# Kernel tuning notes

Hardware: AMD Instinct MI355X
Metric: run time of the kernel (lower is better)

Reference implementation:

```python
import jax, jax.numpy as jnp
import numpy as np

CONF_THRES = 0.25
IOU_THRES = 0.45
MAX_DET = 300
MAX_WH = 4096.0  # class offset for class-aware (non-agnostic) NMS
B, N, NC = 16, 25200, 80


def setup_inputs() -> dict:
    key = jax.random.key(0)
    k1, k2 = jax.random.split(key)
    p = jax.random.uniform(k1, (B, N, 5 + NC), dtype=jnp.float32)
    # scale to realistic YOLO pixel-space xywh for a 640x640 image
    cx = p[..., 0] * 640.0
    cy = p[..., 1] * 640.0
    w = p[..., 2] * 96.0 + 4.0
    h = p[..., 3] * 96.0 + 4.0
    obj = p[..., 4]
    cls = p[..., 5:] * 0.9
    prediction = jnp.concatenate([jnp.stack([cx, cy, w, h, obj], axis=-1), cls], axis=-1)
    logits = jax.random.normal(k2, (B, N, NC), dtype=jnp.float32)
    return {"prediction": prediction, "logits": logits}


def xywh2xyxy(b):
    cx, cy, w, h = b[..., 0], b[..., 1], b[..., 2], b[..., 3]
    return jnp.stack([cx - w * 0.5, cy - h * 0.5, cx + w * 0.5, cy + h * 0.5], axis=-1)


def _iou_one_vs_all(box, boxes):
    # box: [4], boxes: [N,4] in xyxy
    lt = jnp.maximum(box[:2], boxes[:, :2])
    rb = jnp.minimum(box[2:], boxes[:, 2:])
    wh = jnp.clip(rb - lt, 0.0)
    inter = wh[:, 0] * wh[:, 1]
    a1 = (box[2] - box[0]) * (box[3] - box[1])
    a2 = (boxes[:, 2] - boxes[:, 0]) * (boxes[:, 3] - boxes[:, 1])
    return inter / (a1 + a2 - inter + 1e-9)


def _nms_image(x6, boxes_off, scores, log_):
    # greedy NMS, fixed MAX_DET iterations; suppressed/invalid scores are -1
    def step(s, _):
        best = jnp.argmax(s)
        keep = s[best] > 0.0
        iou = _iou_one_vs_all(boxes_off[best], boxes_off)
        s = jnp.where(iou > IOU_THRES, -1.0, s)  # also suppresses 'best' (IoU=1)
        return s, (best, keep)
    _, (idx, keep) = jax.lax.scan(step, scores, None, length=MAX_DET)
    km = keep.astype(x6.dtype)[:, None]
    dets = x6[idx] * km          # [MAX_DET, 6] zero-padded
    lg = log_[idx] * km          # [MAX_DET, 80]
    return dets, lg, keep


def reference(prediction, logits):
    obj = prediction[..., 4]                          # [B,N]
    cls_conf = prediction[..., 5:] * obj[..., None]   # x[:,5:] *= x[:,4:5]
    conf = jnp.max(cls_conf, axis=-1)                 # best class conf
    j = jnp.argmax(cls_conf, axis=-1)                 # best class index
    box = xywh2xyxy(prediction[..., :4])              # [B,N,4]
    valid = (obj > CONF_THRES) & (conf > CONF_THRES)
    scores = jnp.where(valid, conf, -1.0)
    boxes_off = box + (j.astype(box.dtype) * MAX_WH)[..., None]  # class-aware offset
    x6 = jnp.concatenate([box, conf[..., None], j.astype(box.dtype)[..., None]], axis=-1)
    dets, lg, keep = jax.vmap(_nms_image)(x6, boxes_off, scores, logits)
    return dets, lg, keep
```

## Files before the change

kernel.cpp:

```cpp
#include <hip/hip_runtime.h>
#include <cstdint>

#define BB 16
#define NN 25200
#define NCLS 80
#define ROW 85
#define MAXDET 300
#define HBINS 2048
#define CAP2 512
#define TGT 448
#define CONF_T 0.25f
#define IOU_T 0.45f
#define NT 1024

typedef float f4u __attribute__((ext_vector_type(4), aligned(4)));

static const size_t OFF_REC = 1612800;

__global__ __launch_bounds__(256) void k_pre(const float* __restrict__ pred,
                                             float* __restrict__ scoreArr,
                                             float4* __restrict__ recG) {
    int tid = threadIdx.x;
    int t = tid & 3;
    int row = blockIdx.x * 64 + (tid >> 2);
    const float* rp = pred + (size_t)row * ROW;
    float obj = rp[4];
    float best = -1.0f; int bc = 1 << 20;
    f4u c0v;
#pragma unroll
    for (int i = 0; i < 6; ++i) {
        int jj = t + 4 * i;
        if (jj < 21) {
            f4u v4 = *reinterpret_cast<const f4u*>(rp + 4 * jj);
            if (jj == 0) c0v = v4;
            int c0 = 4 * jj;
#pragma unroll
            for (int e = 0; e < 4; ++e) {
                int col = c0 + e;
                if (col >= 5) {
                    float v = __fmul_rn(v4[e], obj);
                    if (v > best) { best = v; bc = col; }
                }
            }
        }
    }
    if (t == 1) {
        float v = __fmul_rn(rp[84], obj);
        if (v > best) { best = v; bc = 84; }
    }
#pragma unroll
    for (int d = 1; d <= 2; d <<= 1) {
        float ob = __shfl_xor(best, d);
        int   oc = __shfl_xor(bc, d);
        if (ob > best || (ob == best && oc < bc)) { best = ob; bc = oc; }
    }
    if (t == 0) {
        bool valid = (obj > CONF_T) && (best > CONF_T);
        scoreArr[row] = valid ? best : -1.0f;
        float cx = c0v[0], cy = c0v[1], w = c0v[2], h = c0v[3];
        float hw = __fmul_rn(w, 0.5f), hh = __fmul_rn(h, 0.5f);
        float4 bb = make_float4(__fsub_rn(cx, hw), __fsub_rn(cy, hh),
                                __fadd_rn(cx, hw), __fadd_rn(cy, hh));
        int bj = bc - 5;
        recG[(size_t)row * 2]     = bb;
        recG[(size_t)row * 2 + 1] = make_float4(__uint_as_float((unsigned)bj), 0.f, 0.f, 0.f);
    }
}

__global__ __launch_bounds__(NT) void k_fused(const float4* __restrict__ recG,
                                              const float* __restrict__ scoreArr,
                                              const float* __restrict__ logits,
                                              float* __restrict__ out) {
    __shared__ union {
        struct { unsigned hist[HBINS]; unsigned csum[257]; } h;
        unsigned long long maskS[CAP2][8];
    } u;
    __shared__ unsigned long long keys[CAP2];
    __shared__ float4 cbox_s[CAP2];
    __shared__ float4 raw_s[CAP2];
    __shared__ unsigned ccls_s[CAP2];
    __shared__ unsigned long long maskT_s[8][64];
    __shared__ unsigned long long keepm_s[8];
    __shared__ unsigned kidx[64];
    __shared__ unsigned rowsrc_s[MAXDET];
    __shared__ int flags[2];
    __shared__ int s_kept;

    int b = blockIdx.x, tid = threadIdx.x;
    int lane = tid & 63;

    for (int k = tid; k < HBINS; k += NT) u.h.hist[k] = 0u;
    if (tid == 0) { flags[0] = 0; flags[1] = 0; }
    __syncthreads();

    float sreg[25];
#pragma unroll
    for (int t = 0; t < 25; ++t) {
        int n = tid + t * NT;
        float s = (n < NN) ? scoreArr[(size_t)b * NN + n] : -1.0f;
        sreg[t] = s;
        if (s > 0.0f) {
            unsigned key = (__float_as_uint(s) - 0x3E800000u) >> 13;
            if (key > HBINS - 1) key = HBINS - 1;
            atomicAdd(&u.h.hist[key], 1u);
        }
    }
    __syncthreads();

    if (tid < 256) {
        unsigned cs = 0;
#pragma unroll
        for (int t = 0; t < 8; ++t) cs += u.h.hist[tid * 8 + t];
        u.h.csum[tid] = cs;
    }
    __syncthreads();
    for (int off = 1; off < 256; off <<= 1) {
        unsigned v = 0, add = 0;
        if (tid < 256) {
            v = u.h.csum[tid];
            add = (tid + off < 256) ? u.h.csum[tid + off] : 0u;
        }
        __syncthreads();
        if (tid < 256) u.h.csum[tid] = v + add;
        __syncthreads();
    }
    if (tid < 256) {
        unsigned Sc = u.h.csum[tid];
        unsigned Sn = (tid < 255) ? u.h.csum[tid + 1] : 0u;
        if (Sc >= TGT && (tid == 255 || Sn < TGT)) {
            unsigned cum = Sn;
            int t = tid * 8;
            for (int k = tid * 8 + 7; k >= tid * 8; --k) {
                cum += u.h.hist[k];
                if (cum >= TGT) { t = k; break; }
            }
            flags[1] = t;
        }
    }
    __syncthreads();
    unsigned thr = (unsigned)flags[1];

#pragma unroll
    for (int t = 0; t < 25; ++t) {
        int n = tid + t * NT;
        float s = sreg[t];
        bool win = false;
        if (s > 0.0f) {
            unsigned key = (__float_as_uint(s) - 0x3E800000u) >> 13;
            if (key > HBINS - 1) key = HBINS - 1;
            win = (key >= thr);
        }
        unsigned long long m = __ballot(win);
        if (m) {
            int lead = __ffsll((long long)m) - 1;
            int base = 0;
            if (lane == lead) base = atomicAdd(&flags[0], __popcll(m));
            base = __shfl(base, lead);
            if (win) {
                int pos = base + __popcll(m & ((1ULL << lane) - 1ULL));
                if (pos < CAP2)
                    keys[pos] = ((unsigned long long)__float_as_uint(s) << 32)
                              | (unsigned long long)(0xFFFFFFFFu - (unsigned)n);
            }
        }
    }
    __syncthreads();
    int c = min(flags[0], CAP2);
    for (int p = tid; p < CAP2; p += NT)
        if (p >= c) keys[p] = 0ULL;
    __syncthreads();

    for (int k = 2; k <= CAP2; k <<= 1) {
        for (int j = k >> 1; j > 0; j >>= 1) {
            for (int i = tid; i < CAP2; i += NT) {
                int ixj = i ^ j;
                if (ixj > i) {
                    unsigned long long k1 = keys[i], k2 = keys[ixj];
                    bool sw = ((i & k) == 0) ? (k1 < k2) : (k1 > k2);
                    if (sw) { keys[i] = k2; keys[ixj] = k1; }
                }
            }
            __syncthreads();
        }
    }

    if (tid < CAP2) {
        int p = tid;
        if (p < c) {
            int n = (int)(0xFFFFFFFFu - (unsigned)keys[p]);
            size_t rb = ((size_t)b * NN + n) * 2;
            float4 bb = recG[rb];
            unsigned bj = __float_as_uint(recG[rb + 1].x);
            raw_s[p] = bb;
            float off = __fmul_rn((float)bj, 4096.0f);
            cbox_s[p] = make_float4(__fadd_rn(bb.x, off), __fadd_rn(bb.y, off),
                                    __fadd_rn(bb.z, off), __fadd_rn(bb.w, off));
            ccls_s[p] = bj;
        } else {
            raw_s[p]  = make_float4(0.f, 0.f, 0.f, 0.f);
            cbox_s[p] = make_float4(0.f, 0.f, 0.f, 0.f);
            ccls_s[p] = 0u;
        }
    }
    __syncthreads();

    for (int k = tid; k < CAP2 * 8; k += NT) {
        int i = k & (CAP2 - 1);
        int w = k >> 9;
        int jbase = w << 6;
        unsigned long long m = 0ULL;
        if (i < c && i < jbase + 63) {
            float4 ci = cbox_s[i];
            float a1 = __fmul_rn(__fsub_rn(ci.z, ci.x), __fsub_rn(ci.w, ci.y));
#pragma unroll 4
            for (int jj = 0; jj < 64; ++jj) {
                int j = jbase + jj;
                float4 cj = cbox_s[j];
                float ltx = fmaxf(ci.x, cj.x), lty = fmaxf(ci.y, cj.y);
                float rbx = fminf(ci.z, cj.z), rby = fminf(ci.w, cj.w);
                float ww = fmaxf(__fsub_rn(rbx, ltx), 0.0f);
                float hh = fmaxf(__fsub_rn(rby, lty), 0.0f);
                float inter = __fmul_rn(ww, hh);
                if (j > i && inter > 0.0f) {
                    float a2 = __fmul_rn(__fsub_rn(cj.z, cj.x), __fsub_rn(cj.w, cj.y));
                    float denom = __fadd_rn(__fsub_rn(__fadd_rn(a1, a2), inter), 1e-9f);
                    if (inter / denom > IOU_T) m |= (1ULL << jj);
                }
            }
        }
        u.maskS[i][w] = m;
    }
    if (tid < 512) {
        int w = tid >> 6, l = tid & 63;
        int jbase = w << 6, p = jbase + l;
        unsigned long long m = 0ULL;
        if (p < c) {
            float4 cl = cbox_s[p];
            float a2 = __fmul_rn(__fsub_rn(cl.z, cl.x), __fsub_rn(cl.w, cl.y));
            for (int ii = 0; ii < 64; ++ii) {
                float4 ci = cbox_s[jbase + ii];
                float ltx = fmaxf(ci.x, cl.x), lty = fmaxf(ci.y, cl.y);
                float rbx = fminf(ci.z, cl.z), rby = fminf(ci.w, cl.w);
                float ww = fmaxf(__fsub_rn(rbx, ltx), 0.0f);
                float hh = fmaxf(__fsub_rn(rby, lty), 0.0f);
                float inter = __fmul_rn(ww, hh);
                if (ii < l && inter > 0.0f) {
                    float a1 = __fmul_rn(__fsub_rn(ci.z, ci.x), __fsub_rn(ci.w, ci.y));
                    float denom = __fadd_rn(__fsub_rn(__fadd_rn(a1, a2), inter), 1e-9f);
                    if (inter / denom > IOU_T) m |= (1ULL << ii);
                }
            }
        }
        maskT_s[w][l] = m;
    }
    __syncthreads();

    if (tid < 64) {
        unsigned long long remq = 0ULL;
        int kept = 0;
        for (int w = 0; w < 8; ++w) {
            int base = w << 6;
            unsigned long long tw = __shfl(remq, w);
            bool pre = ((tw >> lane) & 1ULL) != 0ULL;
            bool validl = (base + lane) < c;
            unsigned long long Cl = maskT_s[w][lane];
            unsigned long long initK = __ballot(validl && !pre);
            unsigned long long K = initK;
            for (int it = 0; it < 64; ++it) {
                bool sup = (Cl & K & ((1ULL << lane) - 1ULL)) != 0ULL;
                unsigned long long K2 = initK & __ballot(!sup);
                if (K2 == K) break;
                K = K2;
            }
            int limit = MAXDET - kept;
            int nk = __popcll(K);
            if (nk > limit) {
                if (limit <= 0) K = 0ULL;
                else {
                    int pref = __popcll(K & ((2ULL << lane) - 1ULL));
                    bool el = ((K >> lane) & 1ULL) && (pref <= limit);
                    K = __ballot(el);
                }
            }
            kept += __popcll(K);
            if (lane == 0) keepm_s[w] = K;
            if (K != 0ULL && w < 7) {
                if ((K >> lane) & 1ULL) {
                    int r = __popcll(K & ((1ULL << lane) - 1ULL));
                    kidx[r] = (unsigned)lane;
                }
                __builtin_amdgcn_s_waitcnt(0);
                int nkk = __popcll(K);
                int q = lane & 7, slot = lane >> 3;
                unsigned long long acc = 0ULL;
                for (int t = slot; t < nkk; t += 8)
                    acc |= u.maskS[base + (int)kidx[t]][q];
                acc |= __shfl_xor(acc, 8);
                acc |= __shfl_xor(acc, 16);
                acc |= __shfl_xor(acc, 32);
                if (slot == 0) remq |= acc;
            }
        }
        if (lane == 0) s_kept = kept;
    }
    __syncthreads();
    int kept = s_kept;

    float* dets = out;
    float* lg   = out + (size_t)BB * MAXDET * 6;
    float* kpo  = lg  + (size_t)BB * MAXDET * NCLS;

    for (int p = tid; p < CAP2; p += NT) {
        if (p < c) {
            int w = p >> 6, bitp = p & 63;
            unsigned long long kw = keepm_s[w];
            if ((kw >> bitp) & 1ULL) {
                int rank = __popcll(kw & ((1ULL << bitp) - 1ULL));
                for (int q = 0; q < w; ++q) rank += __popcll(keepm_s[q]);
                if (rank < MAXDET) {
                    float4 bb = raw_s[p];
                    unsigned long long key = keys[p];
                    float* dr = dets + ((size_t)b * MAXDET + rank) * 6;
                    dr[0] = bb.x; dr[1] = bb.y; dr[2] = bb.z; dr[3] = bb.w;
                    dr[4] = __uint_as_float((unsigned)(key >> 32));
                    dr[5] = (float)ccls_s[p];
                    rowsrc_s[rank] = 0xFFFFFFFFu - (unsigned)key;
                }
            }
        }
    }
    for (int i = tid; i < MAXDET; i += NT) {
        if (i >= kept) {
            float* dr = dets + ((size_t)b * MAXDET + i) * 6;
#pragma unroll
            for (int q = 0; q < 6; ++q) dr[q] = 0.0f;
        }
        kpo[b * MAXDET + i] = (i < kept) ? 1.0f : 0.0f;
    }
    __syncthreads();
    {
        const int HC = NCLS / 2;
        for (int i2 = tid; i2 < MAXDET * HC; i2 += NT) {
            int t = i2 / HC, col2 = i2 - t * HC;
            float2 v = make_float2(0.f, 0.f);
            if (t < kept)
                v = *reinterpret_cast<const float2*>(
                        logits + ((size_t)b * NN + rowsrc_s[t]) * NCLS + col2 * 2);
            *reinterpret_cast<float2*>(
                lg + (size_t)b * MAXDET * NCLS + (size_t)t * NCLS + col2 * 2) = v;
        }
    }
}

extern "C" void kernel_launch(void* const* d_in, const int* in_sizes, int n_in,
                              void* d_out, int out_size, void* d_ws, size_t ws_size,
                              hipStream_t stream) {
    const float* pred   = (const float*)d_in[0];
    const float* logits = (const float*)d_in[1];
    float* out = (float*)d_out;
    char* ws = (char*)d_ws;

    float* scr   = (float*)ws;
    float4* recG = (float4*)(ws + OFF_REC);

    k_pre<<<6300, 256, 0, stream>>>(pred, scr, recG);
    k_fused<<<BB, NT, 0, stream>>>(recG, scr, logits, out);
}
```

Before: 305.0 us.

## Vectorize score loads, register-shuffle bitonic sort, balance IoU mask work, widen stores

```diff
diff --git a/kernel.cpp b/kernel.cpp
--- a/kernel.cpp
+++ b/kernel.cpp
@@ -93,16 +93,27 @@
     if (tid == 0) { flags[0] = 0; flags[1] = 0; }
     __syncthreads();
 
-    float sreg[25];
-#pragma unroll
-    for (int t = 0; t < 25; ++t) {
-        int n = tid + t * NT;
-        float s = (n < NN) ? scoreArr[(size_t)b * NN + n] : -1.0f;
-        sreg[t] = s;
-        if (s > 0.0f) {
-            unsigned key = (__float_as_uint(s) - 0x3E800000u) >> 13;
-            if (key > HBINS - 1) key = HBINS - 1;
-            atomicAdd(&u.h.hist[key], 1u);
+    const float4* sa4 = reinterpret_cast<const float4*>(scoreArr + (size_t)b * NN);
+    f4u sreg[7];
+#pragma unroll
+    for (int t = 0; t < 7; ++t) {
+        int n4 = tid + t * NT;
+        f4u s4;
+        if (n4 < NN / 4) {
+            float4 v = sa4[n4];
+            s4[0] = v.x; s4[1] = v.y; s4[2] = v.z; s4[3] = v.w;
+        } else {
+            s4[0] = s4[1] = s4[2] = s4[3] = -1.0f;
+        }
+        sreg[t] = s4;
+#pragma unroll
+        for (int e = 0; e < 4; ++e) {
+            float s = s4[e];
+            if (s > 0.0f) {
+                unsigned key = (__float_as_uint(s) - 0x3E800000u) >> 13;
+                if (key > HBINS - 1) key = HBINS - 1;
+                atomicAdd(&u.h.hist[key], 1u);
+            }
         }
     }
     __syncthreads();
@@ -141,26 +152,30 @@
     unsigned thr = (unsigned)flags[1];
 
 #pragma unroll
-    for (int t = 0; t < 25; ++t) {
-        int n = tid + t * NT;
-        float s = sreg[t];
-        bool win = false;
-        if (s > 0.0f) {
-            unsigned key = (__float_as_uint(s) - 0x3E800000u) >> 13;
-            if (key > HBINS - 1) key = HBINS - 1;
-            win = (key >= thr);
-        }
-        unsigned long long m = __ballot(win);
-        if (m) {
-            int lead = __ffsll((long long)m) - 1;
-            int base = 0;
-            if (lane == lead) base = atomicAdd(&flags[0], __popcll(m));
-            base = __shfl(base, lead);
-            if (win) {
-                int pos = base + __popcll(m & ((1ULL << lane) - 1ULL));
-                if (pos < CAP2)
-                    keys[pos] = ((unsigned long long)__float_as_uint(s) << 32)
-                              | (unsigned long long)(0xFFFFFFFFu - (unsigned)n);
+    for (int t = 0; t < 7; ++t) {
+        int n4 = tid + t * NT;
+#pragma unroll
+        for (int e = 0; e < 4; ++e) {
+            float s = sreg[t][e];
+            int n = n4 * 4 + e;
+            bool win = false;
+            if (s > 0.0f) {
+                unsigned key = (__float_as_uint(s) - 0x3E800000u) >> 13;
+                if (key > HBINS - 1) key = HBINS - 1;
+                win = (key >= thr);
+            }
+            unsigned long long m = __ballot(win);
+            if (m) {
+                int lead = __ffsll((long long)m) - 1;
+                int base = 0;
+                if (lane == lead) base = atomicAdd(&flags[0], __popcll(m));
+                base = __shfl(base, lead);
+                if (win) {
+                    int pos = base + __popcll(m & ((1ULL << lane) - 1ULL));
+                    if (pos < CAP2)
+                        keys[pos] = ((unsigned long long)__float_as_uint(s) << 32)
+                                  | (unsigned long long)(0xFFFFFFFFu - (unsigned)n);
+                }
             }
         }
     }
@@ -170,18 +185,30 @@
         if (p >= c) keys[p] = 0ULL;
     __syncthreads();
 
-    for (int k = 2; k <= CAP2; k <<= 1) {
-        for (int j = k >> 1; j > 0; j >>= 1) {
-            for (int i = tid; i < CAP2; i += NT) {
-                int ixj = i ^ j;
-                if (ixj > i) {
-                    unsigned long long k1 = keys[i], k2 = keys[ixj];
-                    bool sw = ((i & k) == 0) ? (k1 < k2) : (k1 > k2);
-                    if (sw) { keys[i] = k2; keys[ixj] = k1; }
-                }
-            }
-            __syncthreads();
-        }
+    {
+        unsigned long long key = 0ULL;
+        if (tid < CAP2) key = keys[tid];
+        for (int k = 2; k <= CAP2; k <<= 1) {
+            for (int j = k >> 1; j > 0; j >>= 1) {
+                unsigned long long pr;
+                if (j >= 64) {
+                    __syncthreads();
+                    if (tid < CAP2) keys[tid] = key;
+                    __syncthreads();
+                    pr = (tid < CAP2) ? keys[tid ^ j] : 0ULL;
+                } else {
+                    pr = __shfl_xor(key, j);
+                }
+                if (tid < CAP2) {
+                    bool takemax = (((tid & j) == 0) == ((tid & k) == 0));
+                    bool gt = key > pr;
+                    key = (takemax == gt) ? key : pr;
+                }
+            }
+        }
+        __syncthreads();
+        if (tid < CAP2) keys[tid] = key;
+        __syncthreads();
     }
 
     if (tid < CAP2) {
@@ -204,31 +231,36 @@
     }
     __syncthreads();
 
-    for (int k = tid; k < CAP2 * 8; k += NT) {
-        int i = k & (CAP2 - 1);
-        int w = k >> 9;
-        int jbase = w << 6;
-        unsigned long long m = 0ULL;
-        if (i < c && i < jbase + 63) {
-            float4 ci = cbox_s[i];
-            float a1 = __fmul_rn(__fsub_rn(ci.z, ci.x), __fsub_rn(ci.w, ci.y));
+    for (int h = tid; h < CAP2 * 4; h += NT) {
+        int i0 = h & (CAP2 - 1);
+        int w0 = h >> 9;
+#pragma unroll
+        for (int s = 0; s < 2; ++s) {
+            int i = s ? (CAP2 - 1 - i0) : i0;
+            int w = s ? (7 - w0) : w0;
+            int jbase = w << 6;
+            unsigned long long m = 0ULL;
+            if (i < c && i < jbase + 63) {
+                float4 ci = cbox_s[i];
+                float a1 = __fmul_rn(__fsub_rn(ci.z, ci.x), __fsub_rn(ci.w, ci.y));
 #pragma unroll 4
-            for (int jj = 0; jj < 64; ++jj) {
-                int j = jbase + jj;
-                float4 cj = cbox_s[j];
-                float ltx = fmaxf(ci.x, cj.x), lty = fmaxf(ci.y, cj.y);
-                float rbx = fminf(ci.z, cj.z), rby = fminf(ci.w, cj.w);
-                float ww = fmaxf(__fsub_rn(rbx, ltx), 0.0f);
-                float hh = fmaxf(__fsub_rn(rby, lty), 0.0f);
-                float inter = __fmul_rn(ww, hh);
-                if (j > i && inter > 0.0f) {
-                    float a2 = __fmul_rn(__fsub_rn(cj.z, cj.x), __fsub_rn(cj.w, cj.y));
-                    float denom = __fadd_rn(__fsub_rn(__fadd_rn(a1, a2), inter), 1e-9f);
-                    if (inter / denom > IOU_T) m |= (1ULL << jj);
-                }
-            }
-        }
-        u.maskS[i][w] = m;
+                for (int jj = 0; jj < 64; ++jj) {
+                    int j = jbase + jj;
+                    float4 cj = cbox_s[j];
+                    float ltx = fmaxf(ci.x, cj.x), lty = fmaxf(ci.y, cj.y);
+                    float rbx = fminf(ci.z, cj.z), rby = fminf(ci.w, cj.w);
+                    float ww = fmaxf(__fsub_rn(rbx, ltx), 0.0f);
+                    float hh = fmaxf(__fsub_rn(rby, lty), 0.0f);
+                    float inter = __fmul_rn(ww, hh);
+                    if (j > i && inter > 0.0f) {
+                        float a2 = __fmul_rn(__fsub_rn(cj.z, cj.x), __fsub_rn(cj.w, cj.y));
+                        float denom = __fadd_rn(__fsub_rn(__fadd_rn(a1, a2), inter), 1e-9f);
+                        if (inter / denom > IOU_T) m |= (1ULL << jj);
+                    }
+                }
+            }
+            u.maskS[i][w] = m;
+        }
     }
     if (tid < 512) {
         int w = tid >> 6, l = tid & 63;
@@ -320,10 +352,12 @@
                 if (rank < MAXDET) {
                     float4 bb = raw_s[p];
                     unsigned long long key = keys[p];
-                    float* dr = dets + ((size_t)b * MAXDET + rank) * 6;
-                    dr[0] = bb.x; dr[1] = bb.y; dr[2] = bb.z; dr[3] = bb.w;
-                    dr[4] = __uint_as_float((unsigned)(key >> 32));
-                    dr[5] = (float)ccls_s[p];
+                    float2* dr2 = reinterpret_cast<float2*>(
+                        dets + ((size_t)b * MAXDET + rank) * 6);
+                    dr2[0] = make_float2(bb.x, bb.y);
+                    dr2[1] = make_float2(bb.z, bb.w);
+                    dr2[2] = make_float2(__uint_as_float((unsigned)(key >> 32)),
+                                         (float)ccls_s[p]);
                     rowsrc_s[rank] = 0xFFFFFFFFu - (unsigned)key;
                 }
             }
@@ -331,23 +365,25 @@
     }
     for (int i = tid; i < MAXDET; i += NT) {
         if (i >= kept) {
-            float* dr = dets + ((size_t)b * MAXDET + i) * 6;
-#pragma unroll
-            for (int q = 0; q < 6; ++q) dr[q] = 0.0f;
+            float2* dr2 = reinterpret_cast<float2*>(
+                dets + ((size_t)b * MAXDET + i) * 6);
+            dr2[0] = make_float2(0.f, 0.f);
+            dr2[1] = make_float2(0.f, 0.f);
+            dr2[2] = make_float2(0.f, 0.f);
         }
         kpo[b * MAXDET + i] = (i < kept) ? 1.0f : 0.0f;
     }
     __syncthreads();
     {
-        const int HC = NCLS / 2;
-        for (int i2 = tid; i2 < MAXDET * HC; i2 += NT) {
-            int t = i2 / HC, col2 = i2 - t * HC;
-            float2 v = make_float2(0.f, 0.f);
+        const int QC = NCLS / 4;
+        for (int i4 = tid; i4 < MAXDET * QC; i4 += NT) {
+            int t = i4 / QC, c4 = i4 - t * QC;
+            float4 v = make_float4(0.f, 0.f, 0.f, 0.f);
             if (t < kept)
-                v = *reinterpret_cast<const float2*>(
-                        logits + ((size_t)b * NN + rowsrc_s[t]) * NCLS + col2 * 2);
-            *reinterpret_cast<float2*>(
-                lg + (size_t)b * MAXDET * NCLS + (size_t)t * NCLS + col2 * 2) = v;
+                v = *reinterpret_cast<const float4*>(
+                        logits + ((size_t)b * NN + rowsrc_s[t]) * NCLS + c4 * 4);
+            *reinterpret_cast<float4*>(
+                lg + (size_t)b * MAXDET * NCLS + (size_t)t * NCLS + c4 * 4) = v;
         }
     }
 }
```

Measured after the change: 290.8 us. 1.05x faster.
